# Optimization experiments

Measured on AMD Instinct MI355X. Metric: run time of the kernel, lower is better.

The kernel has to match this reference:

```python
import jax, jax.numpy as jnp
import numpy as np

B, N, F, H, STEPS = 4, 256, 128, 256, 6


def setup_inputs() -> dict:
    key = jax.random.key(0)
    ks = jax.random.split(key, 12)
    s1 = 1.0 / np.sqrt(2 * F + 1)   # fan_in of message_net layer 1
    s2 = 1.0 / np.sqrt(H)           # fan_in of message_net layer 2
    sg = 1.0 / np.sqrt(F)           # GRUCell init scale (1/sqrt(hidden_size))
    u = lambda k, shape, s: jax.random.uniform(k, shape, jnp.float32, -s, s)
    return {
        "x": jax.random.normal(ks[0], (B, N, F), jnp.float32),
        "adj": jax.random.uniform(ks[1], (B, N, N), jnp.float32),
        "mask": jnp.ones((B, N), jnp.float32),
        "W1": u(ks[2], (H, 2 * F + 1), s1),
        "b1": u(ks[3], (H,), s1),
        "W2": u(ks[4], (H, H), s2),
        "b2": u(ks[5], (H,), s2),
        "Wih": u(ks[6], (3 * F, H), sg),
        "bih": u(ks[7], (3 * F,), sg),
        "Whh": u(ks[8], (3 * F, F), sg),
        "bhh": u(ks[9], (3 * F,), sg),
    }


def reference(x, adj, mask, W1, b1, W2, b2, Wih, bih, Whh, bhh):
    Fd = x.shape[-1]
    # Split layer-1 weight over the concat [h_i, h_j, adj_ij] so we never
    # materialize the (B,N,N,2F+1) concat tensor; linearity makes this exact.
    W1i, W1j, w1e = W1[:, :Fd], W1[:, Fd:2 * Fd], W1[:, 2 * Fd]
    valid = ((adj > 0) & (mask[:, None, :] > 0) & (mask[:, :, None] > 0))
    valid = valid.astype(x.dtype)[..., None]  # (B,N,N,1)
    h = x
    for _ in range(STEPS):
        pre = (jnp.einsum('bif,hf->bih', h, W1i)[:, :, None, :]
               + jnp.einsum('bjf,hf->bjh', h, W1j)[:, None, :, :]
               + adj[..., None] * w1e + b1)                 # (B,N,N,H)
        msg = jnp.einsum('bijk,hk->bijh', jax.nn.relu(pre), W2) + b2
        agg = jnp.sum(msg * valid, axis=2)                   # (B,N,H)
        # GRUCell: input=agg (H), hidden=h (F); torch gate order [r, z, n]
        gi = agg @ Wih.T + bih                               # (B,N,3F)
        gh = h @ Whh.T + bhh                                 # (B,N,3F)
        ir, iz, in_ = jnp.split(gi, 3, axis=-1)
        hr, hz, hn = jnp.split(gh, 3, axis=-1)
        r = jax.nn.sigmoid(ir + hr)
        z = jax.nn.sigmoid(iz + hz)
        n = jnp.tanh(in_ + r * hn)
        h = (1.0 - z) * n + z * h
        h = h * mask[..., None]
    return h
```

## Files before the change

### kernel.cpp

```cpp
#include <hip/hip_runtime.h>
#include <hip/hip_bf16.h>

#define BB 4
#define NN 256
#define FD 128
#define HH 256
#define G3 384
#define STEPS 6
#define PO 896
#define NODES (BB*NN)

typedef __hip_bfloat16 bf16;

__device__ float g_h[NODES*FD];
__device__ float g_proj[2*NODES*PO];
__device__ float g_av2[NODES*2*NN];
__device__ float g_deg[NODES];
__device__ float g_mask[NODES];
__device__ float g_PT[FD*PO];
__device__ float g_pbias[PO];
__device__ float g_w1e[HH];
__device__ float g_WihT[HH*G3];
__device__ float g_MT[HH*G3];
__device__ float g_bv[G3];
__device__ float g_bihf[G3];

__device__ __forceinline__ float b2f(bf16 v){ return __bfloat162float(v); }
__device__ __forceinline__ float ldin(const void* p, int i, int isb){
  return isb ? b2f(((const bf16*)p)[i]) : ((const float*)p)[i];
}
__device__ __forceinline__ int probe_bf16(const void* mask){
  return ((const unsigned short*)mask)[0] == 0x3F80 ? 1 : 0;
}

__global__ __launch_bounds__(256) void k_init_a(
    const void* __restrict__ x, const void* __restrict__ adj,
    const void* __restrict__ mask, const void* __restrict__ W1,
    const void* __restrict__ b1, const void* __restrict__ Wih,
    const void* __restrict__ Whh, const void* __restrict__ bhh){
  int isb = probe_bf16(mask);
  int blk = blockIdx.x, tid = threadIdx.x;
  if (blk < 1024){
    int node = blk, b = node >> 8, j = tid;
    float mi = ldin(mask, node, isb);
    float mj = ldin(mask, b*NN + j, isb);
    float a  = ldin(adj, node*NN + j, isb);
    float valid = (a > 0.f && mj > 0.f && mi > 0.f) ? 1.f : 0.f;
    int grp = node >> 2, r = node & 3;
    g_av2[grp*2048 + j*8 + r*2]     = a;
    g_av2[grp*2048 + j*8 + r*2 + 1] = valid;
    __shared__ float red[4];
    float s = valid;
    #pragma unroll
    for (int o = 32; o > 0; o >>= 1) s += __shfl_down(s, o, 64);
    if ((j & 63) == 0) red[j >> 6] = s;
    __syncthreads();
    if (j == 0){ g_deg[node] = red[0]+red[1]+red[2]+red[3]; g_mask[node] = mi; }
    return;
  }
  if (blk < 1472){
    int i = (blk - 1024)*256 + tid;
    int f = i / PO, o = i % PO;
    float v;
    if (o < 256)       v = ldin(W1, o*257 + f, isb);
    else if (o < 512)  v = ldin(W1, (o-256)*257 + FD + f, isb);
    else               v = ldin(Whh, (o-512)*FD + f, isb);
    g_PT[i] = v;
    return;
  }
  if (blk < 1728){
    int h2 = blk - 1472;
    for (int g = tid; g < G3; g += 256)
      g_WihT[h2*G3 + g] = ldin(Wih, g*HH + h2, isb);
    return;
  }
  if (blk < 2240){
    int i = (blk - 1728)*256 + tid;
    g_h[i] = ldin(x, i, isb);
    return;
  }
  for (int i = tid; i < PO; i += 256){
    float v = 0.f;
    if (i < 256) v = ldin(b1, i, isb);
    else if (i >= 512) v = ldin(bhh, i-512, isb);
    g_pbias[i] = v;
  }
  for (int i = tid; i < HH; i += 256) g_w1e[i] = ldin(W1, i*257 + 256, isb);
  for (int i = tid; i < G3; i += 256) g_bihf[i] = 0.f;
}

__global__ __launch_bounds__(384) void k_init_MT(const void* __restrict__ W2,
                                                 const void* __restrict__ b2,
                                                 const void* __restrict__ bih,
                                                 const void* __restrict__ mask){
  int isb = probe_bf16(mask);
  int k = blockIdx.x;
  int g = threadIdx.x;
  __shared__ float col[HH];
  if (g < HH){
    col[g] = (k < HH) ? ldin(W2, g*HH + k, isb) : ldin(b2, g, isb);
  }
  __syncthreads();
  const float* wp = g_WihT + g;
  float a0 = 0.f, a1 = 0.f, a2 = 0.f, a3 = 0.f;
  #pragma unroll 8
  for (int h2 = 0; h2 < HH; h2 += 4){
    a0 = fmaf(col[h2+0], wp[(h2+0)*G3], a0);
    a1 = fmaf(col[h2+1], wp[(h2+1)*G3], a1);
    a2 = fmaf(col[h2+2], wp[(h2+2)*G3], a2);
    a3 = fmaf(col[h2+3], wp[(h2+3)*G3], a3);
  }
  float acc = (a0 + a1) + (a2 + a3);
  if (k < HH){
    g_MT[k*G3 + g] = acc;
  } else {
    g_bv[g] = acc;
    g_bihf[g] = ldin(bih, g, isb);
  }
}

__global__ __launch_bounds__(512) void k_step(void* __restrict__ out,
                                              const void* __restrict__ mask,
                                              int first, int last,
                                              int roff, int woff){
  int grp = blockIdx.x, tid = threadIdx.x, n0 = grp*4;
  __shared__ __align__(16) float Ssh[4][HH];
  __shared__ __align__(16) float hsh[4][FD];
  __shared__ __align__(16) char uni[47104];
  float*  avsh  = (float*)uni;
  float2 (*red)[4][128]  = (float2 (*)[4][128])(uni + 8192);
  float  (*part)[4][G3]  = (float  (*)[4][G3])uni;
  float  (*Aa)[G3]       = (float  (*)[G3])(uni + 24576);
  float  (*Bs)[FD]       = (float  (*)[FD])(uni + 30720);
  float4 (*ppart)[224]   = (float4 (*)[224])(uni + 32768);
  const float* projr = g_proj + roff;
  float*       projw = g_proj + woff;

  if (!first){
    int hp = tid & 127;
    int q  = tid >> 7;
    int b = grp >> 6;
    ((float4*)avsh)[tid] = ((const float4*)(g_av2 + grp*2048))[tid];
    float2 w12 = ((const float2*)g_w1e)[hp];
    float2 Ai2[4], acc2[4];
    #pragma unroll
    for (int r = 0; r < 4; ++r){
      Ai2[r] = *(const float2*)(projr + (n0+r)*PO + 2*hp);
      acc2[r] = make_float2(0.f, 0.f);
    }
    __syncthreads();
    const float* ajp = projr + (b*NN + q*64)*PO + 256 + 2*hp;
    const float4* avp = ((const float4*)avsh) + q*128;
    #pragma unroll 4
    for (int j = 0; j < 64; ++j){
      float2 a2 = *(const float2*)ajp; ajp += PO;
      float4 av01 = avp[2*j];
      float4 av23 = avp[2*j+1];
      float adv[4] = {av01.x, av01.z, av23.x, av23.z};
      float vmv[4] = {av01.y, av01.w, av23.y, av23.w};
      #pragma unroll
      for (int r = 0; r < 4; ++r){
        float vx = Ai2[r].x + a2.x;
        float vy = Ai2[r].y + a2.y;
        vx = fmaf(adv[r], w12.x, vx);
        vy = fmaf(adv[r], w12.y, vy);
        vx = fmaxf(vx, 0.f); vy = fmaxf(vy, 0.f);
        acc2[r].x = fmaf(vx, vmv[r], acc2[r].x);
        acc2[r].y = fmaf(vy, vmv[r], acc2[r].y);
      }
    }
    if (q){
      #pragma unroll
      for (int r = 0; r < 4; ++r) red[q-1][r][hp] = acc2[r];
    }
    __syncthreads();
    if (q == 0){
      #pragma unroll
      for (int r = 0; r < 4; ++r){
        float2 s = acc2[r];
        float2 p0 = red[0][r][hp], p1 = red[1][r][hp], p2 = red[2][r][hp];
        s.x += p0.x + p1.x + p2.x;
        s.y += p0.y + p1.y + p2.y;
        ((float2*)&Ssh[r][0])[hp] = s;
      }
    }
    __syncthreads();

    if (tid < 384){
      int c = tid % 96, sub = tid / 96;
      int k0 = sub*64;
      float4 acc[4];
      #pragma unroll
      for (int r = 0; r < 4; ++r) acc[r] = make_float4(0.f,0.f,0.f,0.f);
      const float4* MT4 = (const float4*)g_MT;
      #pragma unroll 4
      for (int k = 0; k < 64; ++k){
        float4 m = MT4[(k0+k)*96 + c];
        #pragma unroll
        for (int r = 0; r < 4; ++r){
          float s = Ssh[r][k0+k];
          acc[r].x = fmaf(s, m.x, acc[r].x);
          acc[r].y = fmaf(s, m.y, acc[r].y);
          acc[r].z = fmaf(s, m.z, acc[r].z);
          acc[r].w = fmaf(s, m.w, acc[r].w);
        }
      }
      #pragma unroll
      for (int r = 0; r < 4; ++r) ((float4*)&part[sub][r][0])[c] = acc[r];
    }
    __syncthreads();
    if (tid < 384){
      int g = tid;
      float bvg = g_bv[g], bihg = g_bihf[g];
      #pragma unroll
      for (int r = 0; r < 4; ++r){
        float gi = part[0][r][g] + part[1][r][g] + part[2][r][g] + part[3][r][g]
                 + g_deg[n0+r]*bvg + bihg;
        float gh = projr[(n0+r)*PO + 512 + g];
        if (g < 256) Aa[r][g] = gi + gh;
        else { Aa[r][g] = gi; Bs[r][g-256] = gh; }
      }
    }
    __syncthreads();
    if (tid < 128){
      int f = tid, isb = probe_bf16(mask);
      #pragma unroll
      for (int r = 0; r < 4; ++r){
        int node = n0 + r;
        float rr = 1.f/(1.f + __expf(-Aa[r][f]));
        float zz = 1.f/(1.f + __expf(-Aa[r][128+f]));
        float hn = Bs[r][f];
        float narg = Aa[r][256+f] + rr*hn;
        float e = __expf(2.f*narg);
        float nn = 1.f - 2.f/(e + 1.f);
        float hp_ = g_h[node*FD + f];
        float hv = (1.f - zz)*nn + zz*hp_;
        hv *= g_mask[node];
        hsh[r][f] = hv;
        g_h[node*FD + f] = hv;
        if (last){
          if (isb) ((bf16*)out)[node*FD + f] = __float2bfloat16(hv);
          else     ((float*)out)[node*FD + f] = hv;
        }
      }
    }
    __syncthreads();
  } else {
    if (tid < 128) ((float4*)&hsh[0][0])[tid] = ((const float4*)(g_h + n0*FD))[tid];
    __syncthreads();
  }

  if (!last){
    int c = tid & 255, fh = tid >> 8;
    float4 acc[4];
    #pragma unroll
    for (int r = 0; r < 4; ++r) acc[r] = make_float4(0.f,0.f,0.f,0.f);
    if (c < 224){
      const float4* PT4 = (const float4*)g_PT + fh*64*224 + c;
      #pragma unroll 4
      for (int f = 0; f < 64; ++f){
        float4 w = *PT4; PT4 += 224;
        #pragma unroll
        for (int r = 0; r < 4; ++r){
          float hv = hsh[r][fh*64 + f];
          acc[r].x = fmaf(hv, w.x, acc[r].x);
          acc[r].y = fmaf(hv, w.y, acc[r].y);
          acc[r].z = fmaf(hv, w.z, acc[r].z);
          acc[r].w = fmaf(hv, w.w, acc[r].w);
        }
      }
      if (fh == 1){
        #pragma unroll
        for (int r = 0; r < 4; ++r) ppart[r][c] = acc[r];
      }
    }
    __syncthreads();
    if (fh == 0 && c < 224){
      float4 pb = ((const float4*)g_pbias)[c];
      #pragma unroll
      for (int r = 0; r < 4; ++r){
        float4 p = ppart[r][c];
        float4 res;
        res.x = acc[r].x + p.x + pb.x;
        res.y = acc[r].y + p.y + pb.y;
        res.z = acc[r].z + p.z + pb.z;
        res.w = acc[r].w + p.w + pb.w;
        ((float4*)(projw + (n0+r)*PO))[c] = res;
      }
    }
  }
}

extern "C" void kernel_launch(void* const* d_in, const int* in_sizes, int n_in,
                              void* d_out, int out_size, void* d_ws, size_t ws_size,
                              hipStream_t stream){
  (void)in_sizes; (void)n_in; (void)out_size; (void)d_ws; (void)ws_size;
  const void* x    = d_in[0];
  const void* adj  = d_in[1];
  const void* mask = d_in[2];
  const void* W1   = d_in[3];
  const void* b1   = d_in[4];
  const void* W2   = d_in[5];
  const void* b2   = d_in[6];
  const void* Wih  = d_in[7];
  const void* bih  = d_in[8];
  const void* Whh  = d_in[9];
  const void* bhh  = d_in[10];

  k_init_a<<<2241, 256, 0, stream>>>(x, adj, mask, W1, b1, Wih, Whh, bhh);
  k_init_MT<<<HH + 1, 384, 0, stream>>>(W2, b2, bih, mask);

  for (int s = 0; s <= STEPS; ++s){
    int woff = (s & 1) * NODES * PO;
    int roff = ((s + 1) & 1) * NODES * PO;
    k_step<<<NODES/4, 512, 0, stream>>>(d_out, mask, s == 0 ? 1 : 0,
                                        s == STEPS ? 1 : 0, roff, woff);
  }
}
```

Before: 226.6 us.

## Fuse per-step launches into one persistent cooperative kernel with grid sync

Replaces the seven separate k_step launches with a single cooperative kernel that loops over all steps and uses grid.sync() between them. Per-block constants (adjacency/valid values in shared memory, degree, mask, biases, bf16 probe) are loaded once before the loop instead of once per step. The goal is to remove launch overhead and repeated setup loads. In exchange it depends on all 256 blocks of 512 threads being co-resident, and the grid-wide barrier costs something at each step.

```diff
diff --git a/kernel.cpp b/kernel.cpp
--- a/kernel.cpp
+++ b/kernel.cpp
@@ -1,5 +1,8 @@
 #include <hip/hip_runtime.h>
 #include <hip/hip_bf16.h>
+#include <hip/hip_cooperative_groups.h>
+
+namespace cg = cooperative_groups;
 
 #define BB 4
 #define NN 256
@@ -119,174 +122,185 @@
   }
 }
 
-__global__ __launch_bounds__(512) void k_step(void* __restrict__ out,
-                                              const void* __restrict__ mask,
-                                              int first, int last,
-                                              int roff, int woff){
+__global__ __launch_bounds__(512) void k_steps(void* __restrict__ out,
+                                               const void* __restrict__ mask){
+  cg::grid_group grid = cg::this_grid();
   int grp = blockIdx.x, tid = threadIdx.x, n0 = grp*4;
   __shared__ __align__(16) float Ssh[4][HH];
   __shared__ __align__(16) float hsh[4][FD];
+  __shared__ __align__(16) float avs[NN*8];
   __shared__ __align__(16) char uni[47104];
-  float*  avsh  = (float*)uni;
   float2 (*red)[4][128]  = (float2 (*)[4][128])(uni + 8192);
   float  (*part)[4][G3]  = (float  (*)[4][G3])uni;
   float  (*Aa)[G3]       = (float  (*)[G3])(uni + 24576);
   float  (*Bs)[FD]       = (float  (*)[FD])(uni + 30720);
   float4 (*ppart)[224]   = (float4 (*)[224])(uni + 32768);
-  const float* projr = g_proj + roff;
-  float*       projw = g_proj + woff;
-
-  if (!first){
-    int hp = tid & 127;
-    int q  = tid >> 7;
-    int b = grp >> 6;
-    ((float4*)avsh)[tid] = ((const float4*)(g_av2 + grp*2048))[tid];
-    float2 w12 = ((const float2*)g_w1e)[hp];
-    float2 Ai2[4], acc2[4];
-    #pragma unroll
-    for (int r = 0; r < 4; ++r){
-      Ai2[r] = *(const float2*)(projr + (n0+r)*PO + 2*hp);
-      acc2[r] = make_float2(0.f, 0.f);
-    }
-    __syncthreads();
-    const float* ajp = projr + (b*NN + q*64)*PO + 256 + 2*hp;
-    const float4* avp = ((const float4*)avsh) + q*128;
-    #pragma unroll 4
-    for (int j = 0; j < 64; ++j){
-      float2 a2 = *(const float2*)ajp; ajp += PO;
-      float4 av01 = avp[2*j];
-      float4 av23 = avp[2*j+1];
-      float adv[4] = {av01.x, av01.z, av23.x, av23.z};
-      float vmv[4] = {av01.y, av01.w, av23.y, av23.w};
+
+  int isb = probe_bf16(mask);
+  int hp = tid & 127;
+  int q  = tid >> 7;
+  int bb = grp >> 6;
+  float2 w12 = ((const float2*)g_w1e)[hp];
+  int c96 = tid % 96, sub = tid / 96;
+  float bvg = 0.f, bihg = 0.f;
+  if (tid < G3){ bvg = g_bv[tid]; bihg = g_bihf[tid]; }
+  float deg4[4], msk4[4];
+  #pragma unroll
+  for (int r = 0; r < 4; ++r){ deg4[r] = g_deg[n0+r]; msk4[r] = g_mask[n0+r]; }
+  int c = tid & 255, fh = tid >> 8;
+  float4 pb = make_float4(0.f,0.f,0.f,0.f);
+  if (c < 224) pb = ((const float4*)g_pbias)[c];
+  ((float4*)avs)[tid] = ((const float4*)(g_av2 + grp*2048))[tid];
+  __syncthreads();
+
+  for (int s = 0; s <= STEPS; ++s){
+    const float* projr = g_proj + ((s+1)&1)*(NODES*PO);
+    float*       projw = g_proj + (s&1)*(NODES*PO);
+    int last = (s == STEPS);
+
+    if (s){
+      float2 Ai2[4], acc2[4];
       #pragma unroll
       for (int r = 0; r < 4; ++r){
-        float vx = Ai2[r].x + a2.x;
-        float vy = Ai2[r].y + a2.y;
-        vx = fmaf(adv[r], w12.x, vx);
-        vy = fmaf(adv[r], w12.y, vy);
-        vx = fmaxf(vx, 0.f); vy = fmaxf(vy, 0.f);
-        acc2[r].x = fmaf(vx, vmv[r], acc2[r].x);
-        acc2[r].y = fmaf(vy, vmv[r], acc2[r].y);
-      }
+        Ai2[r] = *(const float2*)(projr + (n0+r)*PO + 2*hp);
+        acc2[r] = make_float2(0.f, 0.f);
+      }
+      const float* ajp = projr + (bb*NN + q*64)*PO + 256 + 2*hp;
+      const float4* avp = ((const float4*)avs) + q*128;
+      #pragma unroll 4
+      for (int j = 0; j < 64; ++j){
+        float2 a2 = *(const float2*)ajp; ajp += PO;
+        float4 av01 = avp[2*j];
+        float4 av23 = avp[2*j+1];
+        float adv[4] = {av01.x, av01.z, av23.x, av23.z};
+        float vmv[4] = {av01.y, av01.w, av23.y, av23.w};
+        #pragma unroll
+        for (int r = 0; r < 4; ++r){
+          float vx = Ai2[r].x + a2.x;
+          float vy = Ai2[r].y + a2.y;
+          vx = fmaf(adv[r], w12.x, vx);
+          vy = fmaf(adv[r], w12.y, vy);
+          vx = fmaxf(vx, 0.f); vy = fmaxf(vy, 0.f);
+          acc2[r].x = fmaf(vx, vmv[r], acc2[r].x);
+          acc2[r].y = fmaf(vy, vmv[r], acc2[r].y);
+        }
+      }
+      if (q){
+        #pragma unroll
+        for (int r = 0; r < 4; ++r) red[q-1][r][hp] = acc2[r];
+      }
+      __syncthreads();
+      if (q == 0){
+        #pragma unroll
+        for (int r = 0; r < 4; ++r){
+          float2 sv = acc2[r];
+          float2 p0 = red[0][r][hp], p1 = red[1][r][hp], p2 = red[2][r][hp];
+          sv.x += p0.x + p1.x + p2.x;
+          sv.y += p0.y + p1.y + p2.y;
+          ((float2*)&Ssh[r][0])[hp] = sv;
+        }
+      }
+      __syncthreads();
+
+      if (tid < 384){
+        int k0 = sub*64;
+        float4 acc[4];
+        #pragma unroll
+        for (int r = 0; r < 4; ++r) acc[r] = make_float4(0.f,0.f,0.f,0.f);
+        const float4* MT4 = (const float4*)g_MT;
+        #pragma unroll 4
+        for (int k = 0; k < 64; ++k){
+          float4 m = MT4[(k0+k)*96 + c96];
+          #pragma unroll
+          for (int r = 0; r < 4; ++r){
+            float sv = Ssh[r][k0+k];
+            acc[r].x = fmaf(sv, m.x, acc[r].x);
+            acc[r].y = fmaf(sv, m.y, acc[r].y);
+            acc[r].z = fmaf(sv, m.z, acc[r].z);
+            acc[r].w = fmaf(sv, m.w, acc[r].w);
+          }
+        }
+        #pragma unroll
+        for (int r = 0; r < 4; ++r) ((float4*)&part[sub][r][0])[c96] = acc[r];
+      }
+      __syncthreads();
+      if (tid < 384){
+        int g = tid;
+        #pragma unroll
+        for (int r = 0; r < 4; ++r){
+          float gi = part[0][r][g] + part[1][r][g] + part[2][r][g] + part[3][r][g]
+                   + deg4[r]*bvg + bihg;
+          float gh = projr[(n0+r)*PO + 512 + g];
+          if (g < 256) Aa[r][g] = gi + gh;
+          else { Aa[r][g] = gi; Bs[r][g-256] = gh; }
+        }
+      }
+      __syncthreads();
+      if (tid < 128){
+        int f = tid;
+        #pragma unroll
+        for (int r = 0; r < 4; ++r){
+          int node = n0 + r;
+          float rr = 1.f/(1.f + __expf(-Aa[r][f]));
+          float zz = 1.f/(1.f + __expf(-Aa[r][128+f]));
+          float hn = Bs[r][f];
+          float narg = Aa[r][256+f] + rr*hn;
+          float e = __expf(2.f*narg);
+          float nn = 1.f - 2.f/(e + 1.f);
+          float hp_ = g_h[node*FD + f];
+          float hv = (1.f - zz)*nn + zz*hp_;
+          hv *= msk4[r];
+          hsh[r][f] = hv;
+          g_h[node*FD + f] = hv;
+          if (last){
+            if (isb) ((bf16*)out)[node*FD + f] = __float2bfloat16(hv);
+            else     ((float*)out)[node*FD + f] = hv;
+          }
+        }
+      }
+      __syncthreads();
+    } else {
+      if (tid < 128) ((float4*)&hsh[0][0])[tid] = ((const float4*)(g_h + n0*FD))[tid];
+      __syncthreads();
     }
-    if (q){
-      #pragma unroll
-      for (int r = 0; r < 4; ++r) red[q-1][r][hp] = acc2[r];
-    }
-    __syncthreads();
-    if (q == 0){
-      #pragma unroll
-      for (int r = 0; r < 4; ++r){
-        float2 s = acc2[r];
-        float2 p0 = red[0][r][hp], p1 = red[1][r][hp], p2 = red[2][r][hp];
-        s.x += p0.x + p1.x + p2.x;
-        s.y += p0.y + p1.y + p2.y;
-        ((float2*)&Ssh[r][0])[hp] = s;
-      }
-    }
-    __syncthreads();
-
-    if (tid < 384){
-      int c = tid % 96, sub = tid / 96;
-      int k0 = sub*64;
+
+    if (!last){
       float4 acc[4];
       #pragma unroll
       for (int r = 0; r < 4; ++r) acc[r] = make_float4(0.f,0.f,0.f,0.f);
-      const float4* MT4 = (const float4*)g_MT;
-      #pragma unroll 4
-      for (int k = 0; k < 64; ++k){
-        float4 m = MT4[(k0+k)*96 + c];
-        #pragma unroll
-        for (int r = 0; r < 4; ++r){
-          float s = Ssh[r][k0+k];
-          acc[r].x = fmaf(s, m.x, acc[r].x);
-          acc[r].y = fmaf(s, m.y, acc[r].y);
-          acc[r].z = fmaf(s, m.z, acc[r].z);
-          acc[r].w = fmaf(s, m.w, acc[r].w);
-        }
-      }
-      #pragma unroll
-      for (int r = 0; r < 4; ++r) ((float4*)&part[sub][r][0])[c] = acc[r];
-    }
-    __syncthreads();
-    if (tid < 384){
-      int g = tid;
-      float bvg = g_bv[g], bihg = g_bihf[g];
-      #pragma unroll
-      for (int r = 0; r < 4; ++r){
-        float gi = part[0][r][g] + part[1][r][g] + part[2][r][g] + part[3][r][g]
-                 + g_deg[n0+r]*bvg + bihg;
-        float gh = projr[(n0+r)*PO + 512 + g];
-        if (g < 256) Aa[r][g] = gi + gh;
-        else { Aa[r][g] = gi; Bs[r][g-256] = gh; }
-      }
-    }
-    __syncthreads();
-    if (tid < 128){
-      int f = tid, isb = probe_bf16(mask);
-      #pragma unroll
-      for (int r = 0; r < 4; ++r){
-        int node = n0 + r;
-        float rr = 1.f/(1.f + __expf(-Aa[r][f]));
-        float zz = 1.f/(1.f + __expf(-Aa[r][128+f]));
-        float hn = Bs[r][f];
-        float narg = Aa[r][256+f] + rr*hn;
-        float e = __expf(2.f*narg);
-        float nn = 1.f - 2.f/(e + 1.f);
-        float hp_ = g_h[node*FD + f];
-        float hv = (1.f - zz)*nn + zz*hp_;
-        hv *= g_mask[node];
-        hsh[r][f] = hv;
-        g_h[node*FD + f] = hv;
-        if (last){
-          if (isb) ((bf16*)out)[node*FD + f] = __float2bfloat16(hv);
-          else     ((float*)out)[node*FD + f] = hv;
-        }
-      }
-    }
-    __syncthreads();
-  } else {
-    if (tid < 128) ((float4*)&hsh[0][0])[tid] = ((const float4*)(g_h + n0*FD))[tid];
-    __syncthreads();
-  }
-
-  if (!last){
-    int c = tid & 255, fh = tid >> 8;
-    float4 acc[4];
-    #pragma unroll
-    for (int r = 0; r < 4; ++r) acc[r] = make_float4(0.f,0.f,0.f,0.f);
-    if (c < 224){
-      const float4* PT4 = (const float4*)g_PT + fh*64*224 + c;
-      #pragma unroll 4
-      for (int f = 0; f < 64; ++f){
-        float4 w = *PT4; PT4 += 224;
-        #pragma unroll
-        for (int r = 0; r < 4; ++r){
-          float hv = hsh[r][fh*64 + f];
-          acc[r].x = fmaf(hv, w.x, acc[r].x);
-          acc[r].y = fmaf(hv, w.y, acc[r].y);
-          acc[r].z = fmaf(hv, w.z, acc[r].z);
-          acc[r].w = fmaf(hv, w.w, acc[r].w);
-        }
-      }
-      if (fh == 1){
-        #pragma unroll
-        for (int r = 0; r < 4; ++r) ppart[r][c] = acc[r];
-      }
-    }
-    __syncthreads();
-    if (fh == 0 && c < 224){
-      float4 pb = ((const float4*)g_pbias)[c];
-      #pragma unroll
-      for (int r = 0; r < 4; ++r){
-        float4 p = ppart[r][c];
-        float4 res;
-        res.x = acc[r].x + p.x + pb.x;
-        res.y = acc[r].y + p.y + pb.y;
-        res.z = acc[r].z + p.z + pb.z;
-        res.w = acc[r].w + p.w + pb.w;
-        ((float4*)(projw + (n0+r)*PO))[c] = res;
-      }
+      if (c < 224){
+        const float4* PT4 = (const float4*)g_PT + fh*64*224 + c;
+        #pragma unroll 4
+        for (int f = 0; f < 64; ++f){
+          float4 w = *PT4; PT4 += 224;
+          #pragma unroll
+          for (int r = 0; r < 4; ++r){
+            float hv = hsh[r][fh*64 + f];
+            acc[r].x = fmaf(hv, w.x, acc[r].x);
+            acc[r].y = fmaf(hv, w.y, acc[r].y);
+            acc[r].z = fmaf(hv, w.z, acc[r].z);
+            acc[r].w = fmaf(hv, w.w, acc[r].w);
+          }
+        }
+        if (fh == 1){
+          #pragma unroll
+          for (int r = 0; r < 4; ++r) ppart[r][c] = acc[r];
+        }
+      }
+      __syncthreads();
+      if (fh == 0 && c < 224){
+        #pragma unroll
+        for (int r = 0; r < 4; ++r){
+          float4 p = ppart[r][c];
+          float4 res;
+          res.x = acc[r].x + p.x + pb.x;
+          res.y = acc[r].y + p.y + pb.y;
+          res.z = acc[r].z + p.z + pb.z;
+          res.w = acc[r].w + p.w + pb.w;
+          ((float4*)(projw + (n0+r)*PO))[c] = res;
+        }
+      }
+      grid.sync();
     }
   }
 }
@@ -310,10 +324,9 @@
   k_init_a<<<2241, 256, 0, stream>>>(x, adj, mask, W1, b1, Wih, Whh, bhh);
   k_init_MT<<<HH + 1, 384, 0, stream>>>(W2, b2, bih, mask);
 
-  for (int s = 0; s <= STEPS; ++s){
-    int woff = (s & 1) * NODES * PO;
-    int roff = ((s + 1) & 1) * NODES * PO;
-    k_step<<<NODES/4, 512, 0, stream>>>(d_out, mask, s == 0 ? 1 : 0,
-                                        s == STEPS ? 1 : 0, roff, woff);
-  }
-}
+  void* outp = d_out;
+  const void* maskp = mask;
+  void* args[2] = { (void*)&outp, (void*)&maskp };
+  hipLaunchCooperativeKernel((const void*)k_steps, dim3(NODES/4), dim3(512),
+                             args, 0, stream);
+}
```

Result: slower. 476.6 us (+110.3%).

## Halve nodes per step block and fold first projection into init kernel

Applied to the files above, without the earlier changes.

Each step block now handles 2 nodes instead of 4, so each step launches 512 blocks of 512 threads instead of 256. The aim is to fill more compute units on the GPU and shorten each block's dependent chain. The initial projection of x, previously done by a separate first-step launch, is now computed by extra blocks in k_init_MT, which removes one kernel launch. The trade-off is that the MT and PT weight matrices are streamed by twice as many blocks, roughly doubling L2/global read traffic per step, and each block reuses each loaded weight across fewer nodes.

```diff
diff --git a/kernel.cpp b/kernel.cpp
--- a/kernel.cpp
+++ b/kernel.cpp
@@ -46,9 +46,9 @@
     float mj = ldin(mask, b*NN + j, isb);
     float a  = ldin(adj, node*NN + j, isb);
     float valid = (a > 0.f && mj > 0.f && mi > 0.f) ? 1.f : 0.f;
-    int grp = node >> 2, r = node & 3;
-    g_av2[grp*2048 + j*8 + r*2]     = a;
-    g_av2[grp*2048 + j*8 + r*2 + 1] = valid;
+    int g2 = node >> 1, r2 = node & 1;
+    g_av2[g2*1024 + j*4 + r2*2]     = a;
+    g_av2[g2*1024 + j*4 + r2*2 + 1] = valid;
     __shared__ float red[4];
     float s = valid;
     #pragma unroll
@@ -86,7 +86,6 @@
     g_pbias[i] = v;
   }
   for (int i = tid; i < HH; i += 256) g_w1e[i] = ldin(W1, i*257 + 256, isb);
-  for (int i = tid; i < G3; i += 256) g_bihf[i] = 0.f;
 }
 
 __global__ __launch_bounds__(384) void k_init_MT(const void* __restrict__ W2,
@@ -97,196 +96,211 @@
   int k = blockIdx.x;
   int g = threadIdx.x;
   __shared__ float col[HH];
-  if (g < HH){
-    col[g] = (k < HH) ? ldin(W2, g*HH + k, isb) : ldin(b2, g, isb);
-  }
-  __syncthreads();
-  const float* wp = g_WihT + g;
-  float a0 = 0.f, a1 = 0.f, a2 = 0.f, a3 = 0.f;
-  #pragma unroll 8
-  for (int h2 = 0; h2 < HH; h2 += 4){
-    a0 = fmaf(col[h2+0], wp[(h2+0)*G3], a0);
-    a1 = fmaf(col[h2+1], wp[(h2+1)*G3], a1);
-    a2 = fmaf(col[h2+2], wp[(h2+2)*G3], a2);
-    a3 = fmaf(col[h2+3], wp[(h2+3)*G3], a3);
-  }
-  float acc = (a0 + a1) + (a2 + a3);
-  if (k < HH){
-    g_MT[k*G3 + g] = acc;
-  } else {
-    g_bv[g] = acc;
-    g_bihf[g] = ldin(bih, g, isb);
-  }
-}
-
-__global__ __launch_bounds__(512) void k_step(void* __restrict__ out,
-                                              const void* __restrict__ mask,
-                                              int first, int last,
-                                              int roff, int woff){
-  int grp = blockIdx.x, tid = threadIdx.x, n0 = grp*4;
-  __shared__ __align__(16) float Ssh[4][HH];
-  __shared__ __align__(16) float hsh[4][FD];
-  __shared__ __align__(16) char uni[47104];
-  float*  avsh  = (float*)uni;
-  float2 (*red)[4][128]  = (float2 (*)[4][128])(uni + 8192);
-  float  (*part)[4][G3]  = (float  (*)[4][G3])uni;
-  float  (*Aa)[G3]       = (float  (*)[G3])(uni + 24576);
-  float  (*Bs)[FD]       = (float  (*)[FD])(uni + 30720);
-  float4 (*ppart)[224]   = (float4 (*)[224])(uni + 32768);
+  __shared__ float h2[2][FD];
+  if (k < 257){
+    if (g < HH){
+      col[g] = (k < HH) ? ldin(W2, g*HH + k, isb) : ldin(b2, g, isb);
+    }
+    __syncthreads();
+    const float* wp = g_WihT + g;
+    float a0 = 0.f, a1 = 0.f, a2 = 0.f, a3 = 0.f;
+    #pragma unroll 8
+    for (int h2_ = 0; h2_ < HH; h2_ += 4){
+      a0 = fmaf(col[h2_+0], wp[(h2_+0)*G3], a0);
+      a1 = fmaf(col[h2_+1], wp[(h2_+1)*G3], a1);
+      a2 = fmaf(col[h2_+2], wp[(h2_+2)*G3], a2);
+      a3 = fmaf(col[h2_+3], wp[(h2_+3)*G3], a3);
+    }
+    float acc = (a0 + a1) + (a2 + a3);
+    if (k < HH){
+      g_MT[k*G3 + g] = acc;
+    } else {
+      g_bv[g] = acc;
+      g_bihf[g] = ldin(bih, g, isb);
+    }
+    return;
+  }
+  int n0 = (k - 257)*2;
+  if (g < 64) ((float4*)&h2[0][0])[g] = ((const float4*)(g_h + n0*FD))[g];
+  __syncthreads();
+  if (g < 224){
+    float4 pbv = ((const float4*)g_pbias)[g];
+    float4 a0 = make_float4(0.f,0.f,0.f,0.f), a1 = a0;
+    const float4* PT4 = (const float4*)g_PT + g;
+    #pragma unroll 4
+    for (int f = 0; f < FD; ++f){
+      float4 w = PT4[f*224];
+      float v0 = h2[0][f], v1 = h2[1][f];
+      a0.x = fmaf(v0, w.x, a0.x); a0.y = fmaf(v0, w.y, a0.y);
+      a0.z = fmaf(v0, w.z, a0.z); a0.w = fmaf(v0, w.w, a0.w);
+      a1.x = fmaf(v1, w.x, a1.x); a1.y = fmaf(v1, w.y, a1.y);
+      a1.z = fmaf(v1, w.z, a1.z); a1.w = fmaf(v1, w.w, a1.w);
+    }
+    a0.x += pbv.x; a0.y += pbv.y; a0.z += pbv.z; a0.w += pbv.w;
+    a1.x += pbv.x; a1.y += pbv.y; a1.z += pbv.z; a1.w += pbv.w;
+    ((float4*)(g_proj + n0*PO))[g]     = a0;
+    ((float4*)(g_proj + (n0+1)*PO))[g] = a1;
+  }
+}
+
+__global__ __launch_bounds__(512, 4) void k_step(void* __restrict__ out,
+                                                 const void* __restrict__ mask,
+                                                 int last, int roff, int woff){
+  int grp = blockIdx.x, tid = threadIdx.x, n0 = grp*2;
+  __shared__ __align__(16) float Ssh[2][HH];
+  __shared__ __align__(16) float hsh[2][FD];
+  __shared__ __align__(16) float avs[NN*4];
+  __shared__ __align__(16) char uni[22528];
+  float4 (*red)[2][64]  = (float4 (*)[2][64])uni;
+  float  (*part)[2][G3] = (float  (*)[2][G3])uni;
+  float  (*Aa)[G3]      = (float  (*)[G3])(uni + 16384);
+  float  (*Bs)[FD]      = (float  (*)[FD])(uni + 20480);
+  float4 (*ppart)[224]  = (float4 (*)[224])uni;
+
   const float* projr = g_proj + roff;
   float*       projw = g_proj + woff;
-
-  if (!first){
-    int hp = tid & 127;
-    int q  = tid >> 7;
-    int b = grp >> 6;
-    ((float4*)avsh)[tid] = ((const float4*)(g_av2 + grp*2048))[tid];
-    float2 w12 = ((const float2*)g_w1e)[hp];
-    float2 Ai2[4], acc2[4];
-    #pragma unroll
-    for (int r = 0; r < 4; ++r){
-      Ai2[r] = *(const float2*)(projr + (n0+r)*PO + 2*hp);
-      acc2[r] = make_float2(0.f, 0.f);
-    }
-    __syncthreads();
-    const float* ajp = projr + (b*NN + q*64)*PO + 256 + 2*hp;
-    const float4* avp = ((const float4*)avsh) + q*128;
-    #pragma unroll 4
-    for (int j = 0; j < 64; ++j){
-      float2 a2 = *(const float2*)ajp; ajp += PO;
-      float4 av01 = avp[2*j];
-      float4 av23 = avp[2*j+1];
-      float adv[4] = {av01.x, av01.z, av23.x, av23.z};
-      float vmv[4] = {av01.y, av01.w, av23.y, av23.w};
+  int isb = probe_bf16(mask);
+  int hq = tid & 63;
+  int q  = tid >> 6;
+  int bb = grp >> 7;
+
+  ((float2*)avs)[tid] = ((const float2*)(g_av2 + grp*1024))[tid];
+
+  float4 w14 = ((const float4*)g_w1e)[hq];
+  float4 Ai4[2], acc4[2];
+  #pragma unroll
+  for (int r = 0; r < 2; ++r){
+    Ai4[r] = *(const float4*)(projr + (n0+r)*PO + 4*hq);
+    acc4[r] = make_float4(0.f, 0.f, 0.f, 0.f);
+  }
+  __syncthreads();
+  const float* ajp = projr + (bb*NN + q*32)*PO + 256 + 4*hq;
+  const float4* avp = ((const float4*)avs) + q*32;
+  #pragma unroll 4
+  for (int j = 0; j < 32; ++j){
+    float4 a4 = *(const float4*)ajp; ajp += PO;
+    float4 av = avp[j];
+    float adv[2] = {av.x, av.z};
+    float vmv[2] = {av.y, av.w};
+    #pragma unroll
+    for (int r = 0; r < 2; ++r){
+      float vx = Ai4[r].x + a4.x;
+      float vy = Ai4[r].y + a4.y;
+      float vz = Ai4[r].z + a4.z;
+      float vw = Ai4[r].w + a4.w;
+      vx = fmaf(adv[r], w14.x, vx);
+      vy = fmaf(adv[r], w14.y, vy);
+      vz = fmaf(adv[r], w14.z, vz);
+      vw = fmaf(adv[r], w14.w, vw);
+      vx = fmaxf(vx, 0.f); vy = fmaxf(vy, 0.f);
+      vz = fmaxf(vz, 0.f); vw = fmaxf(vw, 0.f);
+      acc4[r].x = fmaf(vx, vmv[r], acc4[r].x);
+      acc4[r].y = fmaf(vy, vmv[r], acc4[r].y);
+      acc4[r].z = fmaf(vz, vmv[r], acc4[r].z);
+      acc4[r].w = fmaf(vw, vmv[r], acc4[r].w);
+    }
+  }
+  if (q){
+    #pragma unroll
+    for (int r = 0; r < 2; ++r) red[q-1][r][hq] = acc4[r];
+  }
+  __syncthreads();
+  if (q == 0){
+    #pragma unroll
+    for (int r = 0; r < 2; ++r){
+      float4 sv = acc4[r];
       #pragma unroll
-      for (int r = 0; r < 4; ++r){
-        float vx = Ai2[r].x + a2.x;
-        float vy = Ai2[r].y + a2.y;
-        vx = fmaf(adv[r], w12.x, vx);
-        vy = fmaf(adv[r], w12.y, vy);
-        vx = fmaxf(vx, 0.f); vy = fmaxf(vy, 0.f);
-        acc2[r].x = fmaf(vx, vmv[r], acc2[r].x);
-        acc2[r].y = fmaf(vy, vmv[r], acc2[r].y);
+      for (int p = 0; p < 7; ++p){
+        float4 pv = red[p][r][hq];
+        sv.x += pv.x; sv.y += pv.y; sv.z += pv.z; sv.w += pv.w;
       }
-    }
-    if (q){
-      #pragma unroll
-      for (int r = 0; r < 4; ++r) red[q-1][r][hp] = acc2[r];
-    }
-    __syncthreads();
-    if (q == 0){
-      #pragma unroll
-      for (int r = 0; r < 4; ++r){
-        float2 s = acc2[r];
-        float2 p0 = red[0][r][hp], p1 = red[1][r][hp], p2 = red[2][r][hp];
-        s.x += p0.x + p1.x + p2.x;
-        s.y += p0.y + p1.y + p2.y;
-        ((float2*)&Ssh[r][0])[hp] = s;
+      ((float4*)&Ssh[r][0])[hq] = sv;
+    }
+  }
+  __syncthreads();
+
+  if (tid < 384){
+    int c96 = tid % 96, sub = tid / 96;
+    int k0 = sub*64;
+    float4 acc0 = make_float4(0.f,0.f,0.f,0.f), acc1 = acc0;
+    const float4* MT4 = (const float4*)g_MT;
+    #pragma unroll 8
+    for (int k = 0; k < 64; ++k){
+      float4 m = MT4[(k0+k)*96 + c96];
+      float s0 = Ssh[0][k0+k], s1 = Ssh[1][k0+k];
+      acc0.x = fmaf(s0, m.x, acc0.x); acc0.y = fmaf(s0, m.y, acc0.y);
+      acc0.z = fmaf(s0, m.z, acc0.z); acc0.w = fmaf(s0, m.w, acc0.w);
+      acc1.x = fmaf(s1, m.x, acc1.x); acc1.y = fmaf(s1, m.y, acc1.y);
+      acc1.z = fmaf(s1, m.z, acc1.z); acc1.w = fmaf(s1, m.w, acc1.w);
+    }
+    ((float4*)&part[sub][0][0])[c96] = acc0;
+    ((float4*)&part[sub][1][0])[c96] = acc1;
+  }
+  __syncthreads();
+  if (tid < 384){
+    int g = tid;
+    float bvg = g_bv[g], bihg = g_bihf[g];
+    #pragma unroll
+    for (int r = 0; r < 2; ++r){
+      float gi = part[0][r][g] + part[1][r][g] + part[2][r][g] + part[3][r][g]
+               + g_deg[n0+r]*bvg + bihg;
+      float gh = projr[(n0+r)*PO + 512 + g];
+      if (g < 256) Aa[r][g] = gi + gh;
+      else { Aa[r][g] = gi; Bs[r][g-256] = gh; }
+    }
+  }
+  __syncthreads();
+  if (tid < 128){
+    int f = tid;
+    #pragma unroll
+    for (int r = 0; r < 2; ++r){
+      int node = n0 + r;
+      float rr = 1.f/(1.f + __expf(-Aa[r][f]));
+      float zz = 1.f/(1.f + __expf(-Aa[r][128+f]));
+      float hn = Bs[r][f];
+      float narg = Aa[r][256+f] + rr*hn;
+      float e = __expf(2.f*narg);
+      float nn = 1.f - 2.f/(e + 1.f);
+      float hp_ = g_h[node*FD + f];
+      float hv = (1.f - zz)*nn + zz*hp_;
+      hv *= g_mask[node];
+      hsh[r][f] = hv;
+      g_h[node*FD + f] = hv;
+      if (last){
+        if (isb) ((bf16*)out)[node*FD + f] = __float2bfloat16(hv);
+        else     ((float*)out)[node*FD + f] = hv;
       }
     }
-    __syncthreads();
-
-    if (tid < 384){
-      int c = tid % 96, sub = tid / 96;
-      int k0 = sub*64;
-      float4 acc[4];
-      #pragma unroll
-      for (int r = 0; r < 4; ++r) acc[r] = make_float4(0.f,0.f,0.f,0.f);
-      const float4* MT4 = (const float4*)g_MT;
-      #pragma unroll 4
-      for (int k = 0; k < 64; ++k){
-        float4 m = MT4[(k0+k)*96 + c];
-        #pragma unroll
-        for (int r = 0; r < 4; ++r){
-          float s = Ssh[r][k0+k];
-          acc[r].x = fmaf(s, m.x, acc[r].x);
-          acc[r].y = fmaf(s, m.y, acc[r].y);
-          acc[r].z = fmaf(s, m.z, acc[r].z);
-          acc[r].w = fmaf(s, m.w, acc[r].w);
-        }
-      }
-      #pragma unroll
-      for (int r = 0; r < 4; ++r) ((float4*)&part[sub][r][0])[c] = acc[r];
-    }
-    __syncthreads();
-    if (tid < 384){
-      int g = tid;
-      float bvg = g_bv[g], bihg = g_bihf[g];
-      #pragma unroll
-      for (int r = 0; r < 4; ++r){
-        float gi = part[0][r][g] + part[1][r][g] + part[2][r][g] + part[3][r][g]
-                 + g_deg[n0+r]*bvg + bihg;
-        float gh = projr[(n0+r)*PO + 512 + g];
-        if (g < 256) Aa[r][g] = gi + gh;
-        else { Aa[r][g] = gi; Bs[r][g-256] = gh; }
-      }
-    }
-    __syncthreads();
-    if (tid < 128){
-      int f = tid, isb = probe_bf16(mask);
-      #pragma unroll
-      for (int r = 0; r < 4; ++r){
-        int node = n0 + r;
-        float rr = 1.f/(1.f + __expf(-Aa[r][f]));
-        float zz = 1.f/(1.f + __expf(-Aa[r][128+f]));
-        float hn = Bs[r][f];
-        float narg = Aa[r][256+f] + rr*hn;
-        float e = __expf(2.f*narg);
-        float nn = 1.f - 2.f/(e + 1.f);
-        float hp_ = g_h[node*FD + f];
-        float hv = (1.f - zz)*nn + zz*hp_;
-        hv *= g_mask[node];
-        hsh[r][f] = hv;
-        g_h[node*FD + f] = hv;
-        if (last){
-          if (isb) ((bf16*)out)[node*FD + f] = __float2bfloat16(hv);
-          else     ((float*)out)[node*FD + f] = hv;
-        }
-      }
-    }
-    __syncthreads();
-  } else {
-    if (tid < 128) ((float4*)&hsh[0][0])[tid] = ((const float4*)(g_h + n0*FD))[tid];
-    __syncthreads();
-  }
+  }
+  __syncthreads();
 
   if (!last){
     int c = tid & 255, fh = tid >> 8;
-    float4 acc[4];
-    #pragma unroll
-    for (int r = 0; r < 4; ++r) acc[r] = make_float4(0.f,0.f,0.f,0.f);
+    float4 a0 = make_float4(0.f,0.f,0.f,0.f), a1 = a0;
     if (c < 224){
       const float4* PT4 = (const float4*)g_PT + fh*64*224 + c;
       #pragma unroll 4
       for (int f = 0; f < 64; ++f){
         float4 w = *PT4; PT4 += 224;
-        #pragma unroll
-        for (int r = 0; r < 4; ++r){
-          float hv = hsh[r][fh*64 + f];
-          acc[r].x = fmaf(hv, w.x, acc[r].x);
-          acc[r].y = fmaf(hv, w.y, acc[r].y);
-          acc[r].z = fmaf(hv, w.z, acc[r].z);
-          acc[r].w = fmaf(hv, w.w, acc[r].w);
-        }
+        float v0 = hsh[0][fh*64 + f], v1 = hsh[1][fh*64 + f];
+        a0.x = fmaf(v0, w.x, a0.x); a0.y = fmaf(v0, w.y, a0.y);
+        a0.z = fmaf(v0, w.z, a0.z); a0.w = fmaf(v0, w.w, a0.w);
+        a1.x = fmaf(v1, w.x, a1.x); a1.y = fmaf(v1, w.y, a1.y);
+        a1.z = fmaf(v1, w.z, a1.z); a1.w = fmaf(v1, w.w, a1.w);
       }
-      if (fh == 1){
-        #pragma unroll
-        for (int r = 0; r < 4; ++r) ppart[r][c] = acc[r];
-      }
+      if (fh == 1){ ppart[0][c] = a0; ppart[1][c] = a1; }
     }
     __syncthreads();
     if (fh == 0 && c < 224){
-      float4 pb = ((const float4*)g_pbias)[c];
-      #pragma unroll
-      for (int r = 0; r < 4; ++r){
-        float4 p = ppart[r][c];
-        float4 res;
-        res.x = acc[r].x + p.x + pb.x;
-        res.y = acc[r].y + p.y + pb.y;
-        res.z = acc[r].z + p.z + pb.z;
-        res.w = acc[r].w + p.w + pb.w;
-        ((float4*)(projw + (n0+r)*PO))[c] = res;
-      }
+      float4 pbv = ((const float4*)g_pbias)[c];
+      float4 p0 = ppart[0][c], p1 = ppart[1][c];
+      float4 r0, r1;
+      r0.x = a0.x + p0.x + pbv.x; r0.y = a0.y + p0.y + pbv.y;
+      r0.z = a0.z + p0.z + pbv.z; r0.w = a0.w + p0.w + pbv.w;
+      r1.x = a1.x + p1.x + pbv.x; r1.y = a1.y + p1.y + pbv.y;
+      r1.z = a1.z + p1.z + pbv.z; r1.w = a1.w + p1.w + pbv.w;
+      ((float4*)(projw + n0*PO))[c]     = r0;
+      ((float4*)(projw + (n0+1)*PO))[c] = r1;
     }
   }
 }
@@ -308,12 +322,11 @@
   const void* bhh  = d_in[10];
 
   k_init_a<<<2241, 256, 0, stream>>>(x, adj, mask, W1, b1, Wih, Whh, bhh);
-  k_init_MT<<<HH + 1, 384, 0, stream>>>(W2, b2, bih, mask);
-
-  for (int s = 0; s <= STEPS; ++s){
+  k_init_MT<<<257 + 512, 384, 0, stream>>>(W2, b2, bih, mask);
+
+  for (int s = 1; s <= STEPS; ++s){
     int woff = (s & 1) * NODES * PO;
     int roff = ((s + 1) & 1) * NODES * PO;
-    k_step<<<NODES/4, 512, 0, stream>>>(d_out, mask, s == 0 ? 1 : 0,
-                                        s == STEPS ? 1 : 0, roff, woff);
-  }
-}
+    k_step<<<512, 512, 0, stream>>>(d_out, mask, s == STEPS ? 1 : 0, roff, woff);
+  }
+}
```

Measured after the change: 234.3 us. +3.4%, slower.
